# Optimization experiments

Hardware: AMD Instinct MI355X
Metric: run time of the kernel (lower is better)

The kernel has to match this reference:

```python
import jax, jax.numpy as jnp
import numpy as np

VOCAB, D, M = 400000, 50, 128
B, L = 64, 512

def setup_inputs() -> dict:
    key = jax.random.key(0)
    k1, k2, k3, k4, k5, k6 = jax.random.split(key, 6)
    return {
        "x": jax.random.randint(k1, (B, L), 0, VOCAB),
        "amp_table": jax.random.normal(k2, (VOCAB, D), dtype=jnp.float32),
        "pha_table": jax.random.uniform(k3, (VOCAB, D), dtype=jnp.float32) * (2.0 * np.pi),
        "mix_table": jax.random.normal(k4, (VOCAB, 1), dtype=jnp.float32),
        "kernel_real": jax.random.normal(k5, (M, D), dtype=jnp.float32),
        "kernel_imag": jax.random.normal(k6, (M, D), dtype=jnp.float32),
    }

def reference(x, amp_table, pha_table, mix_table, kernel_real, kernel_imag):
    # Embedding lookups: amplitude, phase, and mixture logit per token
    amp = amp_table[x]            # [B, L, D]
    pha = pha_table[x]            # [B, L, D]
    mix = mix_table[x][..., 0]    # [B, L]

    # softmax over sequence dim (dim=1) -> per-token mixture weights
    w = jax.nn.softmax(mix, axis=1)  # [B, L]

    # complex token vector v = amp * exp(i * pha)
    vr = amp * jnp.cos(pha)       # [B, L, D]
    vi = amp * jnp.sin(pha)       # [B, L, D]

    # Fused density + mixture: rho = sum_l w_l * v_l v_l^H  (never materialize [B,L,D,D])
    rho_r = jnp.einsum('bl,bld,ble->bde', w, vr, vr) + jnp.einsum('bl,bld,ble->bde', w, vi, vi)
    rho_i = jnp.einsum('bl,bld,ble->bde', w, vi, vr) - jnp.einsum('bl,bld,ble->bde', w, vr, vi)

    # Row-normalized complex measurement vectors m_k
    norm = jnp.sqrt(jnp.sum(kernel_real**2 + kernel_imag**2, axis=-1, keepdims=True))
    kr = kernel_real / norm       # [M, D]
    ki = kernel_imag / norm       # [M, D]

    # p_k = Re(m_k^H rho m_k); conj(m)_d m_e = (kr_d kr_e + ki_d ki_e) + i(kr_d ki_e - ki_d kr_e)
    p = (jnp.einsum('bde,md,me->bm', rho_r, kr, kr)
         + jnp.einsum('bde,md,me->bm', rho_r, ki, ki)
         - jnp.einsum('bde,md,me->bm', rho_i, kr, ki)
         + jnp.einsum('bde,md,me->bm', rho_i, ki, kr))
    return p                      # [B, M]
```

## Files before the change

kernel.cpp:

```cpp
#include <hip/hip_runtime.h>
#include <math.h>

#define D      50
#define MM     128
#define LL     512
#define BB     64
#define KK     128
#define KS     136
#define LT     64
#define NCH    8
#define NTHREADS 256

typedef __attribute__((ext_vector_type(8))) short  short8;
typedef __attribute__((ext_vector_type(4))) float  float4v;

__device__ __forceinline__ void bsplit(float x, short& hi, short& lo) {
    unsigned u = __float_as_uint(x);
    unsigned r = u + 0x7FFFu + ((u >> 16) & 1u);
    hi = (short)(r >> 16);
    float res = x - __uint_as_float(r & 0xFFFF0000u);
    unsigned u2 = __float_as_uint(res);
    unsigned r2 = u2 + 0x7FFFu + ((u2 >> 16) & 1u);
    lo = (short)(r2 >> 16);
}

__global__ void __launch_bounds__(NTHREADS)
qdnn_prep(const float* __restrict__ kernel_real,
          const float* __restrict__ kernel_imag,
          float* __restrict__ out,
          short* __restrict__ ws_frag,
          float* __restrict__ ws_norm)
{
    const int tid = threadIdx.x;
    if (blockIdx.x == 8) {
        #pragma unroll
        for (int j = 0; j < (BB * MM) / NTHREADS; ++j)
            out[j * NTHREADS + tid] = 0.0f;
        return;
    }
    const int ntile = blockIdx.x;
    const int lane  = tid & 63;
    const int kstep = tid >> 6;
    const int col   = lane & 15;
    const int g     = lane >> 4;
    const int m     = ntile * 16 + col;
    const float* krow = kernel_real + m * D;
    const float* irow = kernel_imag + m * D;

    short8 fr_hi, fr_lo, fi_hi, fi_lo;
    float np = 0.0f;
    #pragma unroll
    for (int j = 0; j < 8; ++j) {
        const int k = kstep * 32 + g * 8 + j;
        float br = 0.0f, bi = 0.0f;
        if (k < D) {
            const float a = krow[k], c = irow[k];
            br = a; bi = -c;
            np = fmaf(a, a, fmaf(c, c, np));
        } else if (k < 2 * D) {
            const float a = krow[k - D], c = irow[k - D];
            br = c; bi = a;
        }
        short h, l;
        bsplit(br, h, l); fr_hi[j] = h; fr_lo[j] = l;
        bsplit(bi, h, l); fi_hi[j] = h; fi_lo[j] = l;
    }
    const size_t fb = (size_t)((ntile * 4 + kstep) * 4) * 64 * 8;
    *(short8*)(ws_frag + fb + (size_t)(0 * 64 + lane) * 8) = fr_hi;
    *(short8*)(ws_frag + fb + (size_t)(1 * 64 + lane) * 8) = fr_lo;
    *(short8*)(ws_frag + fb + (size_t)(2 * 64 + lane) * 8) = fi_hi;
    *(short8*)(ws_frag + fb + (size_t)(3 * 64 + lane) * 8) = fi_lo;

    __shared__ float s_nr[NTHREADS];
    s_nr[tid] = np;
    __syncthreads();
    if (tid < 16) {
        float s = 0.0f;
        #pragma unroll
        for (int u = 0; u < 16; ++u) s += s_nr[tid + 16 * u];
        ws_norm[ntile * 16 + tid] = s;
    }
}

__global__ void __launch_bounds__(NTHREADS)
qdnn_main(const int*   __restrict__ x,
          const float* __restrict__ amp_table,
          const float* __restrict__ pha_table,
          const float* __restrict__ mix_table,
          const short* __restrict__ ws_frag,
          const float* __restrict__ ws_norm,
          float* __restrict__ out)
{
    __shared__ short s_vhi[LT * KS];
    __shared__ short s_vlo[LT * KS];
    __shared__ int   s_x[LL];
    __shared__ float s_w[LL];
    __shared__ float s_red[8];

    const int tid    = threadIdx.x;
    const int b      = blockIdx.x >> 3;
    const int lchunk = blockIdx.x & 7;
    const int wave   = tid >> 6;
    const int lane   = tid & 63;

    const int* xg = x + b * LL;
    s_x[tid]       = xg[tid];
    s_x[tid + 256] = xg[tid + 256];
    __syncthreads();

    const float v0 = mix_table[s_x[tid]];
    const float v1 = mix_table[s_x[tid + 256]];
    float lmax = fmaxf(v0, v1);
    #pragma unroll
    for (int off = 32; off > 0; off >>= 1)
        lmax = fmaxf(lmax, __shfl_down(lmax, off));
    if (lane == 0) s_red[wave] = lmax;
    __syncthreads();
    const float bmax = fmaxf(fmaxf(s_red[0], s_red[1]), fmaxf(s_red[2], s_red[3]));
    const float e0 = __expf(v0 - bmax);
    const float e1 = __expf(v1 - bmax);
    s_w[tid]       = e0;
    s_w[tid + 256] = e1;
    float esum = e0 + e1;
    #pragma unroll
    for (int off = 32; off > 0; off >>= 1)
        esum += __shfl_down(esum, off);
    if (lane == 0) s_red[4 + wave] = esum;
    __syncthreads();
    const float inv = 1.0f / (s_red[4] + s_red[5] + s_red[6] + s_red[7]);
    s_w[tid]       *= inv;
    s_w[tid + 256] *= inv;

    {
        const int tok   = tid >> 2;
        const int dbase = (tid & 3) * 13;
        const int gidx  = s_x[lchunk * LT + tok];
        const float* arow = amp_table + (size_t)gidx * D;
        const float* prow = pha_table + (size_t)gidx * D;
        #pragma unroll
        for (int jj = 0; jj < 13; ++jj) {
            const int d = dbase + jj;
            if (d < D) {
                const float a = arow[d], ph = prow[d];
                float sn, cs;
                __sincosf(ph, &sn, &cs);
                short h, l;
                bsplit(a * cs, h, l);
                s_vhi[tok * KS + d] = h;      s_vlo[tok * KS + d] = l;
                bsplit(a * sn, h, l);
                s_vhi[tok * KS + D + d] = h;  s_vlo[tok * KS + D + d] = l;
            }
        }
        for (int j = tid; j < LT * (KS - 2 * D); j += NTHREADS) {
            const int r = j / (KS - 2 * D);
            const int c = 2 * D + (j - r * (KS - 2 * D));
            s_vhi[r * KS + c] = 0;
            s_vlo[r * KS + c] = 0;
        }
    }
    __syncthreads();

    const int l15 = lane & 15;
    const int g   = lane >> 4;
    for (int miter = 0; miter < 2; ++miter) {
        const int ntile = miter * 4 + wave;
        short8 fr_hi[4], fr_lo[4], fi_hi[4], fi_lo[4];
        #pragma unroll
        for (int ks = 0; ks < 4; ++ks) {
            const size_t fb = (size_t)((ntile * 4 + ks) * 4) * 64 * 8;
            fr_hi[ks] = *(const short8*)(ws_frag + fb + (size_t)(0 * 64 + lane) * 8);
            fr_lo[ks] = *(const short8*)(ws_frag + fb + (size_t)(1 * 64 + lane) * 8);
            fi_hi[ks] = *(const short8*)(ws_frag + fb + (size_t)(2 * 64 + lane) * 8);
            fi_lo[ks] = *(const short8*)(ws_frag + fb + (size_t)(3 * 64 + lane) * 8);
        }
        const float nrm = ws_norm[ntile * 16 + l15];

        float pm = 0.0f;
        for (int liter = 0; liter < 4; ++liter) {
            const int lb = liter * 16;
            float4v ar[4], ai[4];
            #pragma unroll
            for (int ks = 0; ks < 4; ++ks) {
                ar[ks] = (float4v)(0.0f);
                ai[ks] = (float4v)(0.0f);
            }
            #pragma unroll
            for (int ks = 0; ks < 4; ++ks) {
                const int aoff = (lb + l15) * KS + ks * 32 + g * 8;
                const short8 ah = *(const short8*)(s_vhi + aoff);
                const short8 al = *(const short8*)(s_vlo + aoff);
                ar[ks] = __builtin_amdgcn_mfma_f32_16x16x32_bf16(ah, fr_hi[ks], ar[ks], 0, 0, 0);
                ar[ks] = __builtin_amdgcn_mfma_f32_16x16x32_bf16(ah, fr_lo[ks], ar[ks], 0, 0, 0);
                ar[ks] = __builtin_amdgcn_mfma_f32_16x16x32_bf16(al, fr_hi[ks], ar[ks], 0, 0, 0);
                ar[ks] = __builtin_amdgcn_mfma_f32_16x16x32_bf16(al, fr_lo[ks], ar[ks], 0, 0, 0);
                ai[ks] = __builtin_amdgcn_mfma_f32_16x16x32_bf16(ah, fi_hi[ks], ai[ks], 0, 0, 0);
                ai[ks] = __builtin_amdgcn_mfma_f32_16x16x32_bf16(ah, fi_lo[ks], ai[ks], 0, 0, 0);
                ai[ks] = __builtin_amdgcn_mfma_f32_16x16x32_bf16(al, fi_hi[ks], ai[ks], 0, 0, 0);
                ai[ks] = __builtin_amdgcn_mfma_f32_16x16x32_bf16(al, fi_lo[ks], ai[ks], 0, 0, 0);
            }
            #pragma unroll
            for (int reg = 0; reg < 4; ++reg) {
                const float arr = ar[0][reg] + ar[1][reg] + ar[2][reg] + ar[3][reg];
                const float aii = ai[0][reg] + ai[1][reg] + ai[2][reg] + ai[3][reg];
                const float wl  = s_w[lchunk * LT + lb + g * 4 + reg];
                pm = fmaf(wl, fmaf(arr, arr, aii * aii), pm);
            }
        }
        pm += __shfl_xor(pm, 16);
        pm += __shfl_xor(pm, 32);
        if (lane < 16)
            atomicAdd(&out[b * MM + ntile * 16 + l15], pm / nrm);
    }
}

extern "C" void kernel_launch(void* const* d_in, const int* in_sizes, int n_in,
                              void* d_out, int out_size, void* d_ws, size_t ws_size,
                              hipStream_t stream) {
    const int*   xx  = (const int*)d_in[0];
    const float* amp = (const float*)d_in[1];
    const float* pha = (const float*)d_in[2];
    const float* mix = (const float*)d_in[3];
    const float* kr  = (const float*)d_in[4];
    const float* ki  = (const float*)d_in[5];
    float* out = (float*)d_out;

    short* ws_frag = (short*)d_ws;
    float* ws_norm = (float*)((char*)d_ws + 131072);

    hipLaunchKernelGGL(qdnn_prep, dim3(9), dim3(NTHREADS), 0, stream,
                       kr, ki, out, ws_frag, ws_norm);
    hipLaunchKernelGGL(qdnn_main, dim3(BB * NCH), dim3(NTHREADS), 0, stream,
                       xx, amp, pha, mix, ws_frag, ws_norm, out);
}
```

Baseline: 174.5 us.

## Hoist softmax into prep kernel, drop lo*lo MFMA terms, vectorize token staging

Moves the per-batch softmax over the sequence into extra blocks of the prep kernel. Each of the eight L-chunk blocks per batch no longer recomputes it, and the main kernel reads only its 64 weights. Drops the lo×lo bf16 split MFMA products, cutting matrix work by a quarter at a small precision cost. Embedding staging now uses float2 loads and packed 32-bit LDS stores. Loops are unrolled, and the norm divide becomes a multiply by a precomputed reciprocal.

```diff
diff --git a/kernel.cpp b/kernel.cpp
--- a/kernel.cpp
+++ b/kernel.cpp
@@ -5,8 +5,8 @@
 #define MM     128
 #define LL     512
 #define BB     64
-#define KK     128
 #define KS     136
+#define KSU    68
 #define LT     64
 #define NCH    8
 #define NTHREADS 256
@@ -24,61 +24,100 @@
     lo = (short)(r2 >> 16);
 }
 
+__device__ __forceinline__ void bsplit2(float x0, float x1, unsigned& hiU, unsigned& loU) {
+    short h0, l0, h1, l1;
+    bsplit(x0, h0, l0);
+    bsplit(x1, h1, l1);
+    hiU = (unsigned)(unsigned short)h0 | ((unsigned)(unsigned short)h1 << 16);
+    loU = (unsigned)(unsigned short)l0 | ((unsigned)(unsigned short)l1 << 16);
+}
+
 __global__ void __launch_bounds__(NTHREADS)
-qdnn_prep(const float* __restrict__ kernel_real,
+qdnn_prep(const int*   __restrict__ x,
+          const float* __restrict__ mix_table,
+          const float* __restrict__ kernel_real,
           const float* __restrict__ kernel_imag,
           float* __restrict__ out,
           short* __restrict__ ws_frag,
-          float* __restrict__ ws_norm)
+          float* __restrict__ ws_inorm,
+          float* __restrict__ ws_w)
 {
+    __shared__ float s_nr[NTHREADS];
+    __shared__ float s_red[8];
     const int tid = threadIdx.x;
-    if (blockIdx.x == 8) {
+    const int blk = blockIdx.x;
+
+    if (blk < 8) {
+        const int ntile = blk;
+        const int lane  = tid & 63;
+        const int kstep = tid >> 6;
+        const int col   = lane & 15;
+        const int g     = lane >> 4;
+        const int m     = ntile * 16 + col;
+        const float* krow = kernel_real + m * D;
+        const float* irow = kernel_imag + m * D;
+
+        short8 fr_hi, fr_lo, fi_hi, fi_lo;
+        float np = 0.0f;
+        #pragma unroll
+        for (int j = 0; j < 8; ++j) {
+            const int k = kstep * 32 + g * 8 + j;
+            float br = 0.0f, bi = 0.0f;
+            if (k < D) {
+                const float a = krow[k], c = irow[k];
+                br = a; bi = -c;
+                np = fmaf(a, a, fmaf(c, c, np));
+            } else if (k < 2 * D) {
+                const float a = krow[k - D], c = irow[k - D];
+                br = c; bi = a;
+            }
+            short h, l;
+            bsplit(br, h, l); fr_hi[j] = h; fr_lo[j] = l;
+            bsplit(bi, h, l); fi_hi[j] = h; fi_lo[j] = l;
+        }
+        const size_t fb = (size_t)((ntile * 4 + kstep) * 4) * 64 * 8;
+        *(short8*)(ws_frag + fb + (size_t)(0 * 64 + lane) * 8) = fr_hi;
+        *(short8*)(ws_frag + fb + (size_t)(1 * 64 + lane) * 8) = fr_lo;
+        *(short8*)(ws_frag + fb + (size_t)(2 * 64 + lane) * 8) = fi_hi;
+        *(short8*)(ws_frag + fb + (size_t)(3 * 64 + lane) * 8) = fi_lo;
+
+        s_nr[tid] = np;
+        __syncthreads();
+        if (tid < 16) {
+            float s = 0.0f;
+            #pragma unroll
+            for (int u = 0; u < 16; ++u) s += s_nr[tid + 16 * u];
+            ws_inorm[ntile * 16 + tid] = 1.0f / s;
+        }
+    } else if (blk == 8) {
         #pragma unroll
         for (int j = 0; j < (BB * MM) / NTHREADS; ++j)
             out[j * NTHREADS + tid] = 0.0f;
-        return;
-    }
-    const int ntile = blockIdx.x;
-    const int lane  = tid & 63;
-    const int kstep = tid >> 6;
-    const int col   = lane & 15;
-    const int g     = lane >> 4;
-    const int m     = ntile * 16 + col;
-    const float* krow = kernel_real + m * D;
-    const float* irow = kernel_imag + m * D;
-
-    short8 fr_hi, fr_lo, fi_hi, fi_lo;
-    float np = 0.0f;
-    #pragma unroll
-    for (int j = 0; j < 8; ++j) {
-        const int k = kstep * 32 + g * 8 + j;
-        float br = 0.0f, bi = 0.0f;
-        if (k < D) {
-            const float a = krow[k], c = irow[k];
-            br = a; bi = -c;
-            np = fmaf(a, a, fmaf(c, c, np));
-        } else if (k < 2 * D) {
-            const float a = krow[k - D], c = irow[k - D];
-            br = c; bi = a;
-        }
-        short h, l;
-        bsplit(br, h, l); fr_hi[j] = h; fr_lo[j] = l;
-        bsplit(bi, h, l); fi_hi[j] = h; fi_lo[j] = l;
-    }
-    const size_t fb = (size_t)((ntile * 4 + kstep) * 4) * 64 * 8;
-    *(short8*)(ws_frag + fb + (size_t)(0 * 64 + lane) * 8) = fr_hi;
-    *(short8*)(ws_frag + fb + (size_t)(1 * 64 + lane) * 8) = fr_lo;
-    *(short8*)(ws_frag + fb + (size_t)(2 * 64 + lane) * 8) = fi_hi;
-    *(short8*)(ws_frag + fb + (size_t)(3 * 64 + lane) * 8) = fi_lo;
-
-    __shared__ float s_nr[NTHREADS];
-    s_nr[tid] = np;
-    __syncthreads();
-    if (tid < 16) {
-        float s = 0.0f;
-        #pragma unroll
-        for (int u = 0; u < 16; ++u) s += s_nr[tid + 16 * u];
-        ws_norm[ntile * 16 + tid] = s;
+    } else {
+        const int b = blk - 9;
+        const int wave = tid >> 6, lane = tid & 63;
+        const int g0 = x[b * LL + tid];
+        const int g1 = x[b * LL + tid + 256];
+        const float v0 = mix_table[g0];
+        const float v1 = mix_table[g1];
+        float lmax = fmaxf(v0, v1);
+        #pragma unroll
+        for (int off = 32; off > 0; off >>= 1)
+            lmax = fmaxf(lmax, __shfl_down(lmax, off));
+        if (lane == 0) s_red[wave] = lmax;
+        __syncthreads();
+        const float bmax = fmaxf(fmaxf(s_red[0], s_red[1]), fmaxf(s_red[2], s_red[3]));
+        const float e0 = __expf(v0 - bmax);
+        const float e1 = __expf(v1 - bmax);
+        float esum = e0 + e1;
+        #pragma unroll
+        for (int off = 32; off > 0; off >>= 1)
+            esum += __shfl_down(esum, off);
+        if (lane == 0) s_red[4 + wave] = esum;
+        __syncthreads();
+        const float inv = 1.0f / (s_red[4] + s_red[5] + s_red[6] + s_red[7]);
+        ws_w[b * LL + tid]       = e0 * inv;
+        ws_w[b * LL + tid + 256] = e1 * inv;
     }
 }
 
@@ -86,16 +125,14 @@
 qdnn_main(const int*   __restrict__ x,
           const float* __restrict__ amp_table,
           const float* __restrict__ pha_table,
-          const float* __restrict__ mix_table,
           const short* __restrict__ ws_frag,
-          const float* __restrict__ ws_norm,
+          const float* __restrict__ ws_inorm,
+          const float* __restrict__ ws_w,
           float* __restrict__ out)
 {
     __shared__ short s_vhi[LT * KS];
     __shared__ short s_vlo[LT * KS];
-    __shared__ int   s_x[LL];
-    __shared__ float s_w[LL];
-    __shared__ float s_red[8];
+    __shared__ float s_w64[LT];
 
     const int tid    = threadIdx.x;
     const int b      = blockIdx.x >> 3;
@@ -103,65 +140,44 @@
     const int wave   = tid >> 6;
     const int lane   = tid & 63;
 
-    const int* xg = x + b * LL;
-    s_x[tid]       = xg[tid];
-    s_x[tid + 256] = xg[tid + 256];
-    __syncthreads();
-
-    const float v0 = mix_table[s_x[tid]];
-    const float v1 = mix_table[s_x[tid + 256]];
-    float lmax = fmaxf(v0, v1);
-    #pragma unroll
-    for (int off = 32; off > 0; off >>= 1)
-        lmax = fmaxf(lmax, __shfl_down(lmax, off));
-    if (lane == 0) s_red[wave] = lmax;
-    __syncthreads();
-    const float bmax = fmaxf(fmaxf(s_red[0], s_red[1]), fmaxf(s_red[2], s_red[3]));
-    const float e0 = __expf(v0 - bmax);
-    const float e1 = __expf(v1 - bmax);
-    s_w[tid]       = e0;
-    s_w[tid + 256] = e1;
-    float esum = e0 + e1;
-    #pragma unroll
-    for (int off = 32; off > 0; off >>= 1)
-        esum += __shfl_down(esum, off);
-    if (lane == 0) s_red[4 + wave] = esum;
-    __syncthreads();
-    const float inv = 1.0f / (s_red[4] + s_red[5] + s_red[6] + s_red[7]);
-    s_w[tid]       *= inv;
-    s_w[tid + 256] *= inv;
-
     {
-        const int tok   = tid >> 2;
-        const int dbase = (tid & 3) * 13;
-        const int gidx  = s_x[lchunk * LT + tok];
+        const int tok = tid >> 2;
+        const int t4  = tid & 3;
+        const int gidx = x[b * LL + lchunk * LT + tok];
         const float* arow = amp_table + (size_t)gidx * D;
         const float* prow = pha_table + (size_t)gidx * D;
-        #pragma unroll
-        for (int jj = 0; jj < 13; ++jj) {
-            const int d = dbase + jj;
-            if (d < D) {
-                const float a = arow[d], ph = prow[d];
-                float sn, cs;
-                __sincosf(ph, &sn, &cs);
-                short h, l;
-                bsplit(a * cs, h, l);
-                s_vhi[tok * KS + d] = h;      s_vlo[tok * KS + d] = l;
-                bsplit(a * sn, h, l);
-                s_vhi[tok * KS + D + d] = h;  s_vlo[tok * KS + D + d] = l;
-            }
-        }
-        for (int j = tid; j < LT * (KS - 2 * D); j += NTHREADS) {
-            const int r = j / (KS - 2 * D);
-            const int c = 2 * D + (j - r * (KS - 2 * D));
-            s_vhi[r * KS + c] = 0;
-            s_vlo[r * KS + c] = 0;
-        }
+        unsigned* vhiU = (unsigned*)s_vhi;
+        unsigned* vloU = (unsigned*)s_vlo;
+        const int rb = tok * KSU;
+        #pragma unroll
+        for (int j = 0; j < 7; ++j) {
+            const int e = t4 + 4 * j;
+            if (e < 25) {
+                const float2 a2 = *(const float2*)(arow + 2 * e);
+                const float2 p2 = *(const float2*)(prow + 2 * e);
+                float sn0, cs0, sn1, cs1;
+                __sincosf(p2.x, &sn0, &cs0);
+                __sincosf(p2.y, &sn1, &cs1);
+                unsigned hu, lu;
+                bsplit2(a2.x * cs0, a2.y * cs1, hu, lu);
+                vhiU[rb + e] = hu;  vloU[rb + e] = lu;
+                bsplit2(a2.x * sn0, a2.y * sn1, hu, lu);
+                vhiU[rb + 25 + e] = hu;  vloU[rb + 25 + e] = lu;
+            }
+        }
+        for (int j = tid; j < LT * (KSU - 50); j += NTHREADS) {
+            const int r = j / (KSU - 50);
+            const int c = j - r * (KSU - 50);
+            vhiU[r * KSU + 50 + c] = 0;
+            vloU[r * KSU + 50 + c] = 0;
+        }
+        if (tid < LT) s_w64[tid] = ws_w[b * LL + lchunk * LT + tid];
     }
     __syncthreads();
 
     const int l15 = lane & 15;
     const int g   = lane >> 4;
+    #pragma unroll
     for (int miter = 0; miter < 2; ++miter) {
         const int ntile = miter * 4 + wave;
         short8 fr_hi[4], fr_lo[4], fi_hi[4], fi_lo[4];
@@ -173,9 +189,10 @@
             fi_hi[ks] = *(const short8*)(ws_frag + fb + (size_t)(2 * 64 + lane) * 8);
             fi_lo[ks] = *(const short8*)(ws_frag + fb + (size_t)(3 * 64 + lane) * 8);
         }
-        const float nrm = ws_norm[ntile * 16 + l15];
+        const float inrm = ws_inorm[ntile * 16 + l15];
 
         float pm = 0.0f;
+        #pragma unroll
         for (int liter = 0; liter < 4; ++liter) {
             const int lb = liter * 16;
             float4v ar[4], ai[4];
@@ -192,24 +209,22 @@
                 ar[ks] = __builtin_amdgcn_mfma_f32_16x16x32_bf16(ah, fr_hi[ks], ar[ks], 0, 0, 0);
                 ar[ks] = __builtin_amdgcn_mfma_f32_16x16x32_bf16(ah, fr_lo[ks], ar[ks], 0, 0, 0);
                 ar[ks] = __builtin_amdgcn_mfma_f32_16x16x32_bf16(al, fr_hi[ks], ar[ks], 0, 0, 0);
-                ar[ks] = __builtin_amdgcn_mfma_f32_16x16x32_bf16(al, fr_lo[ks], ar[ks], 0, 0, 0);
                 ai[ks] = __builtin_amdgcn_mfma_f32_16x16x32_bf16(ah, fi_hi[ks], ai[ks], 0, 0, 0);
                 ai[ks] = __builtin_amdgcn_mfma_f32_16x16x32_bf16(ah, fi_lo[ks], ai[ks], 0, 0, 0);
                 ai[ks] = __builtin_amdgcn_mfma_f32_16x16x32_bf16(al, fi_hi[ks], ai[ks], 0, 0, 0);
-                ai[ks] = __builtin_amdgcn_mfma_f32_16x16x32_bf16(al, fi_lo[ks], ai[ks], 0, 0, 0);
             }
             #pragma unroll
             for (int reg = 0; reg < 4; ++reg) {
                 const float arr = ar[0][reg] + ar[1][reg] + ar[2][reg] + ar[3][reg];
                 const float aii = ai[0][reg] + ai[1][reg] + ai[2][reg] + ai[3][reg];
-                const float wl  = s_w[lchunk * LT + lb + g * 4 + reg];
+                const float wl  = s_w64[lb + g * 4 + reg];
                 pm = fmaf(wl, fmaf(arr, arr, aii * aii), pm);
             }
         }
         pm += __shfl_xor(pm, 16);
         pm += __shfl_xor(pm, 32);
         if (lane < 16)
-            atomicAdd(&out[b * MM + ntile * 16 + l15], pm / nrm);
+            atomicAdd(&out[b * MM + ntile * 16 + l15], pm * inrm);
     }
 }
 
@@ -224,11 +239,12 @@
     const float* ki  = (const float*)d_in[5];
     float* out = (float*)d_out;
 
-    short* ws_frag = (short*)d_ws;
-    float* ws_norm = (float*)((char*)d_ws + 131072);
-
-    hipLaunchKernelGGL(qdnn_prep, dim3(9), dim3(NTHREADS), 0, stream,
-                       kr, ki, out, ws_frag, ws_norm);
+    short* ws_frag  = (short*)d_ws;
+    float* ws_inorm = (float*)((char*)d_ws + 131072);
+    float* ws_w     = (float*)((char*)d_ws + 131584);
+
+    hipLaunchKernelGGL(qdnn_prep, dim3(9 + BB), dim3(NTHREADS), 0, stream,
+                       xx, mix, kr, ki, out, ws_frag, ws_inorm, ws_w);
     hipLaunchKernelGGL(qdnn_main, dim3(BB * NCH), dim3(NTHREADS), 0, stream,
-                       xx, amp, pha, mix, ws_frag, ws_norm, out);
-}
+                       xx, amp, pha, ws_frag, ws_inorm, ws_w, out);
+}
```

After: 165.0 us. 5.4% less time.
